# Optimization experiments

Measured on AMD Instinct MI355X. Metric: run time of the kernel, lower is better.

Reference implementation:

```python
import jax, jax.numpy as jnp
import numpy as np

NUM_HEADS = 16

def _div_no_nan(num, den):
    # TF divide_no_nan semantics: 0 where denominator is 0
    safe = jnp.where(den == 0, 1.0, den)
    return jnp.where(den == 0, 0.0, num / safe)

def setup_inputs() -> dict:
    key = jax.random.key(0)
    x = jax.random.normal(key, (8, 4096, 1024), dtype=jnp.float32)
    return {"x": x}

def reference(x) -> jnp.ndarray:
    B, S, D = x.shape
    H = NUM_HEADS
    hs = D // H
    # [B, S, H, hs] -> [B, H, S, hs]
    t = x.reshape(B, S, H, hs).transpose(0, 2, 1, 3)
    # count_nonzero over the sequence axis (axis=2 here == axis=1 inside _pca)
    non_zeros = jnp.sum((t != 0).astype(jnp.float32), axis=2, keepdims=True)      # [B,H,1,hs]
    zero_vectors = (jnp.sum((t != 0), axis=-1, keepdims=True) > 0).astype(jnp.float32)  # [B,H,S,1]
    mean_vector = _div_no_nan(jnp.sum(t, axis=2, keepdims=True), non_zeros)       # [B,H,1,hs]
    var_vector = jnp.sum(_div_no_nan(jnp.square(t - mean_vector), non_zeros), axis=2, keepdims=True)
    std_vector = jnp.sqrt(var_vector)                                             # [B,H,1,hs]
    out = _div_no_nan(t - mean_vector, std_vector) * zero_vectors                 # [B,H,S,hs]
    # Gram matrix per (batch, head): [B,H,hs,hs]
    gram = jnp.einsum('bhsi,bhsj->bhij', out, out)
    eigen_values, eigen_vectors = jnp.linalg.eigh(gram)      # [B,H,hs], [B,H,hs,hs]
    # diag(w) @ V then transpose the last two axes
    pca = jnp.swapaxes(eigen_values[..., :, None] * eigen_vectors, -1, -2)        # [B,H,hs,hs]
    pca = pca.reshape(B, H * hs, hs)
    return pca / jnp.sqrt(jnp.asarray(hs, dtype=jnp.float32))
```

## Files before the change

### kernel.cpp

```cpp
#include <hip/hip_runtime.h>
#include <math.h>


#define NMAT 128
#define EPS32 5.9604644775390625e-8
#define SAFMIN32 1.1754943508222875e-38

static __device__ __forceinline__ double f32r(double x) { return (double)(float)x; }
static __device__ __forceinline__ double lapsign(double a, double b) {
  return (b >= 0.0) ? fabs(a) : -fabs(a);
}

__device__ __forceinline__ double wred_sum(double v) {
#pragma unroll
  for (int o = 32; o > 0; o >>= 1) v += __shfl_xor(v, o, 64);
  return v;
}
__device__ __forceinline__ double wred_max(double v) {
#pragma unroll
  for (int o = 32; o > 0; o >>= 1) v = fmax(v, __shfl_xor(v, o, 64));
  return v;
}

__global__ __launch_bounds__(256) void gram_kernel(const float* __restrict__ x,
                                                   float* __restrict__ gbuf) {
  const int bh = blockIdx.x, b = bh >> 4, h = bh & 15;
  const float* base = x + (size_t)b * 4096 * 1024 + h * 64;
  __shared__ double rs1[16][64];
  __shared__ double rs2[16][64];
  __shared__ int rsc[16][64];
  __shared__ float sm[64], si[64];
  __shared__ double tiled[2][64][68];
  const int tid = threadIdx.x, q = tid & 15, r0 = tid >> 4, lane = tid & 63;

  double s1[4] = {0.0, 0.0, 0.0, 0.0}, s2[4] = {0.0, 0.0, 0.0, 0.0};
  int cc[4] = {0, 0, 0, 0};
#pragma unroll 4
  for (int s = r0; s < 4096; s += 16) {
    const float4 v = *(const float4*)&base[(size_t)s * 1024 + 4 * q];
    const float vs[4] = {v.x, v.y, v.z, v.w};
#pragma unroll
    for (int k = 0; k < 4; ++k) {
      const double dv = (double)vs[k];
      s1[k] += dv;
      s2[k] += dv * dv;
      cc[k] += (vs[k] != 0.0f) ? 1 : 0;
    }
  }
#pragma unroll
  for (int k = 0; k < 4; ++k) {
    rs1[r0][4 * q + k] = s1[k];
    rs2[r0][4 * q + k] = s2[k];
    rsc[r0][4 * q + k] = cc[k];
  }
  __syncthreads();
  if (tid < 64) {
    double S1 = 0.0, S2 = 0.0;
    int C = 0;
    for (int a = 0; a < 16; ++a) { S1 += rs1[a][tid]; S2 += rs2[a][tid]; C += rsc[a][tid]; }
    const double m = (C > 0) ? S1 / (double)C : 0.0;
    double var = (C > 0) ? (S2 - 2.0 * m * S1 + 4096.0 * m * m) / (double)C : 0.0;
    var = fmax(var, 0.0);
    const double sd = sqrt(var);
    sm[tid] = (float)m;
    si[tid] = (sd > 0.0) ? (float)(1.0 / sd) : 0.0f;
  }
  __syncthreads();

  const float4 mj4 = *(const float4*)&sm[4 * q];
  const float4 iv4 = *(const float4*)&si[4 * q];

  auto stash = [&](int buf, const float4& v, int sl) {
    const bool nz4 = (v.x != 0.0f) || (v.y != 0.0f) || (v.z != 0.0f) || (v.w != 0.0f);
    const unsigned long long mb = __ballot(nz4);
    const unsigned rowm = (unsigned)(mb >> (lane & 48)) & 0xFFFFu;
    double* tr = &tiled[buf][sl][4 * q];
    if (rowm) {
      tr[0] = (double)((v.x - mj4.x) * iv4.x);
      tr[1] = (double)((v.y - mj4.y) * iv4.y);
      tr[2] = (double)((v.z - mj4.z) * iv4.z);
      tr[3] = (double)((v.w - mj4.w) * iv4.w);
    } else {
      tr[0] = 0.0; tr[1] = 0.0; tr[2] = 0.0; tr[3] = 0.0;
    }
  };

  double acc[4][4];
#pragma unroll
  for (int r = 0; r < 4; ++r)
#pragma unroll
    for (int c = 0; c < 4; ++c) acc[r][c] = 0.0;

  {
    const float4 p0 = *(const float4*)&base[(size_t)(r0) * 1024 + 4 * q];
    const float4 p1 = *(const float4*)&base[(size_t)(r0 + 16) * 1024 + 4 * q];
    const float4 p2 = *(const float4*)&base[(size_t)(r0 + 32) * 1024 + 4 * q];
    const float4 p3 = *(const float4*)&base[(size_t)(r0 + 48) * 1024 + 4 * q];
    stash(0, p0, r0); stash(0, p1, r0 + 16); stash(0, p2, r0 + 32); stash(0, p3, r0 + 48);
  }
  __syncthreads();

  for (int t = 0; t < 64; ++t) {
    const int cur = t & 1;
    float4 n0, n1, n2, n3;
    const bool more = (t + 1 < 64);
    if (more) {
      const size_t sb = (size_t)(t + 1) * 64;
      n0 = *(const float4*)&base[(sb + r0) * 1024 + 4 * q];
      n1 = *(const float4*)&base[(sb + r0 + 16) * 1024 + 4 * q];
      n2 = *(const float4*)&base[(sb + r0 + 32) * 1024 + 4 * q];
      n3 = *(const float4*)&base[(sb + r0 + 48) * 1024 + 4 * q];
    }
    for (int ss = 0; ss < 64; ++ss) {
      const double* ta = &tiled[cur][ss][4 * r0];
      const double* tb = &tiled[cur][ss][4 * q];
      const double a0 = ta[0], a1 = ta[1], a2 = ta[2], a3 = ta[3];
      const double b0 = tb[0], b1 = tb[1], b2 = tb[2], b3 = tb[3];
      acc[0][0] += a0 * b0; acc[0][1] += a0 * b1; acc[0][2] += a0 * b2; acc[0][3] += a0 * b3;
      acc[1][0] += a1 * b0; acc[1][1] += a1 * b1; acc[1][2] += a1 * b2; acc[1][3] += a1 * b3;
      acc[2][0] += a2 * b0; acc[2][1] += a2 * b1; acc[2][2] += a2 * b2; acc[2][3] += a2 * b3;
      acc[3][0] += a3 * b0; acc[3][1] += a3 * b1; acc[3][2] += a3 * b2; acc[3][3] += a3 * b3;
    }
    if (more) {
      stash(cur ^ 1, n0, r0); stash(cur ^ 1, n1, r0 + 16);
      stash(cur ^ 1, n2, r0 + 32); stash(cur ^ 1, n3, r0 + 48);
    }
    __syncthreads();
  }

  float* G = gbuf + (size_t)bh * 4096;
#pragma unroll
  for (int r = 0; r < 4; ++r)
#pragma unroll
    for (int c = 0; c < 4; ++c)
      G[(4 * r0 + r) * 64 + 4 * q + c] = (float)acc[r][c];
}

static __device__ void dlartg_d(double f, double g, double& cs, double& sn,
                                double& r) {
  if (g == 0.0) { cs = 1.0; sn = 0.0; r = f; }
  else if (f == 0.0) { cs = 0.0; sn = 1.0; r = g; }
  else {
    r = sqrt(f * f + g * g);
    cs = f / r; sn = g / r;
    if (fabs(f) > fabs(g) && cs < 0.0) { cs = -cs; sn = -sn; r = -r; }
  }
}

static __device__ void dlaev2_d(double a, double b, double c, double& rt1,
                                double& rt2, double& cs1, double& sn1) {
  double sm = a + c, df = a - c, adf = fabs(df), tb = b + b, ab = fabs(tb);
  double acmx, acmn;
  if (fabs(a) > fabs(c)) { acmx = a; acmn = c; } else { acmx = c; acmn = a; }
  double rt;
  if (adf > ab) rt = adf * sqrt(1.0 + (ab / adf) * (ab / adf));
  else if (adf < ab) rt = ab * sqrt(1.0 + (adf / ab) * (adf / ab));
  else rt = ab * sqrt(2.0);
  int sgn1;
  if (sm < 0.0) {
    rt1 = 0.5 * (sm - rt); sgn1 = -1;
    rt2 = (acmx / rt1) * acmn - (b / rt1) * b;
  } else if (sm > 0.0) {
    rt1 = 0.5 * (sm + rt); sgn1 = 1;
    rt2 = (acmx / rt1) * acmn - (b / rt1) * b;
  } else { rt1 = 0.5 * rt; rt2 = -0.5 * rt; sgn1 = 1; }
  int sgn2; double cs;
  if (df >= 0.0) { cs = df + rt; sgn2 = 1; } else { cs = df - rt; sgn2 = -1; }
  double acs = fabs(cs);
  if (acs > ab) {
    double ct = -tb / cs;
    sn1 = 1.0 / sqrt(1.0 + ct * ct); cs1 = ct * sn1;
  } else {
    if (ab == 0.0) { cs1 = 1.0; sn1 = 0.0; }
    else {
      double tn = -cs / tb;
      cs1 = 1.0 / sqrt(1.0 + tn * tn); sn1 = tn * cs1;
    }
  }
  if (sgn1 == sgn2) { double tn = cs1; cs1 = -sn1; sn1 = tn; }
}

static __device__ void dsteqr16_grp(double (*Zs)[65], int base, int lane,
                                    double& dk, double& ek) {
  const int n = 16, nm1 = 15;
  const double eps = EPS32, eps2 = EPS32 * EPS32;
  const int gb = lane & 48;
  const int row = lane & 15;
  int l1 = 0, jtot = 0, nmaxit = n * 30;
  while (l1 < n) {
    if (l1 > 0) { if (row == l1 - 1) ek = 0.0; }
    int m;
    {
      double dkp1 = __shfl(dk, gb + ((row + 1) & 15));
      bool cond = (fabs(ek) <= (sqrt(fabs(dk)) * sqrt(fabs(dkp1))) * eps);
      unsigned grp = (unsigned)((__ballot(cond) >> gb) & 0xFFFFull);
      grp &= 0x7FFFu & ~((1u << l1) - 1);
      m = grp ? (__ffs(grp) - 1) : nm1;
      if (m < nm1) { if (row == m) ek = 0.0; }
    }
    int l = l1, lend = m;
    l1 = m + 1;
    if (lend == l) continue;
    if (fabs(__shfl(dk, gb + lend)) < fabs(__shfl(dk, gb + l))) {
      int t = l; l = lend; lend = t;
    }
    if (lend > l) {
      for (;;) {
        int mm;
        {
          double dkp1 = __shfl(dk, gb + ((row + 1) & 15));
          bool cond = (ek * ek <= (eps2 * fabs(dk)) * fabs(dkp1) + SAFMIN32);
          unsigned grp = (unsigned)((__ballot(cond) >> gb) & 0xFFFFull);
          unsigned rng = ((1u << lend) - 1) & ~((1u << l) - 1);
          grp &= rng;
          mm = grp ? (__ffs(grp) - 1) : lend;
        }
        if (mm < lend) { if (row == mm) ek = 0.0; }
        double p = __shfl(dk, gb + l);
        if (mm == l) { ++l; if (l <= lend) continue; else break; }
        if (mm == l + 1) {
          double rt1, rt2, c, s;
          dlaev2_d(__shfl(dk, gb + l), __shfl(ek, gb + l),
                   __shfl(dk, gb + l + 1), rt1, rt2, c, s);
          {
            double a = Zs[base + row][base + l], b = Zs[base + row][base + l + 1];
            Zs[base + row][base + l] = c * a + s * b;
            Zs[base + row][base + l + 1] = -s * a + c * b;
          }
          if (row == l) { dk = rt1; ek = 0.0; }
          if (row == l + 1) dk = rt2;
          l += 2; if (l <= lend) continue; else break;
        }
        if (jtot == nmaxit) break;
        ++jtot;
        double el = __shfl(ek, gb + l);
        double g = (__shfl(dk, gb + l + 1) - p) / (2.0 * el);
        double r = sqrt(g * g + 1.0);
        g = __shfl(dk, gb + mm) - p + el / (g + lapsign(r, g));
        double s = 1.0, c = 1.0; p = 0.0;
        double carry = 0.0;
        bool first = true;
        for (int i = mm - 1; i >= l; --i) {
          double za = Zs[base + row][base + i];
          double ei = __shfl(ek, gb + i);
          double f = s * ei, b = c * ei;
          dlartg_d(g, f, c, s, r);
          if (i != mm - 1) { if (row == i + 1) ek = r; }
          g = __shfl(dk, gb + i + 1) - p;
          r = (__shfl(dk, gb + i) - g) * s + 2.0 * c * b;
          p = s * r;
          if (row == i + 1) dk = g + p;
          g = c * r - b;
          double zb = first ? Zs[base + row][base + i + 1] : carry;
          Zs[base + row][base + i + 1] = s * za + c * zb;
          carry = c * za - s * zb;
          first = false;
        }
        Zs[base + row][base + l] = carry;
        if (row == l) { dk -= p; ek = g; }
      }
    } else {
      for (;;) {
        int mm;
        {
          int lm1 = (row == 0) ? 0 : row - 1;
          double dkm1 = __shfl(dk, gb + lm1);
          double ekm1 = __shfl(ek, gb + lm1);
          bool cond = (ekm1 * ekm1 <= (eps2 * fabs(dk)) * fabs(dkm1) + SAFMIN32);
          unsigned grp = (unsigned)((__ballot(cond) >> gb) & 0xFFFFull);
          unsigned rng = ((1u << (l + 1)) - 1) & ~((1u << (lend + 1)) - 1);
          grp &= rng;
          mm = grp ? (31 - __clz(grp)) : lend;
        }
        if (mm > lend) { if (row == mm - 1) ek = 0.0; }
        double p = __shfl(dk, gb + l);
        if (mm == l) { --l; if (l >= lend) continue; else break; }
        if (mm == l - 1) {
          double rt1, rt2, c, s;
          dlaev2_d(__shfl(dk, gb + l - 1), __shfl(ek, gb + l - 1),
                   __shfl(dk, gb + l), rt1, rt2, c, s);
          {
            double a = Zs[base + row][base + l - 1], b = Zs[base + row][base + l];
            Zs[base + row][base + l - 1] = c * a + s * b;
            Zs[base + row][base + l] = -s * a + c * b;
          }
          if (row == l - 1) { dk = rt1; ek = 0.0; }
          if (row == l) dk = rt2;
          l -= 2; if (l >= lend) continue; else break;
        }
        if (jtot == nmaxit) break;
        ++jtot;
        double elm1 = __shfl(ek, gb + l - 1);
        double g = (__shfl(dk, gb + l - 1) - p) / (2.0 * elm1);
        double r = sqrt(g * g + 1.0);
        g = __shfl(dk, gb + mm) - p + elm1 / (g + lapsign(r, g));
        double s = 1.0, c = 1.0; p = 0.0;
        double carry = 0.0;
        bool first = true;
        for (int i = mm; i <= l - 1; ++i) {
          double zb = Zs[base + row][base + i + 1];
          double ei = __shfl(ek, gb + i);
          double f = s * ei, b = c * ei;
          dlartg_d(g, f, c, s, r);
          if (i != mm) { if (row == i - 1) ek = r; }
          g = __shfl(dk, gb + i) - p;
          r = (__shfl(dk, gb + i + 1) - g) * s + 2.0 * c * b;
          p = s * r;
          if (row == i) dk = g + p;
          g = c * r - b;
          double za = first ? Zs[base + row][base + i] : carry;
          Zs[base + row][base + i] = c * za + s * zb;
          carry = -s * za + c * zb;
          first = false;
        }
        Zs[base + row][base + l] = carry;
        if (row == l) dk -= p;
        if (row == l - 1) ek = g;
      }
    }
  }
  for (int ii = 1; ii < n; ++ii) {
    int i = ii - 1;
    double p = __shfl(dk, gb + i);
    double mv = (row >= ii) ? dk : 1.0e300;
    mv = fmin(mv, __shfl_xor(mv, 8));
    mv = fmin(mv, __shfl_xor(mv, 4));
    mv = fmin(mv, __shfl_xor(mv, 2));
    mv = fmin(mv, __shfl_xor(mv, 1));
    if (mv < p) {
      unsigned grp = (unsigned)((__ballot(row >= ii && dk == mv) >> gb) & 0xFFFFull);
      int k = __ffs(grp) - 1;
      double dko = __shfl(dk, gb + k);
      if (row == k) dk = p;
      if (row == i) dk = dko;
      double t = Zs[base + row][base + i];
      Zs[base + row][base + i] = Zs[base + row][base + k];
      Zs[base + row][base + k] = t;
    }
  }
}

static __device__ void merge_dc(int off, int n, double rho_in, int lane,
                                double (*Zs)[65], double (*Zn)[65], float* ScF,
                                double* dd, double* dlam, double* wz,
                                double* zt, double* lamv, double* zloc,
                                double* dloc, double* lamfin, double* dvalS,
                                double* rz2, int* indx, int* slist, int* dlist,
                                int* dcolS) {
  const int N1 = n / 2;
  if (lane < n) {
    int r = (lane < N1) ? (off + N1 - 1) : (off + N1);
    double z = Zs[r][off + lane];
    if (rho_in < 0.0 && lane >= N1) z = -z;
    zloc[lane] = z * 0.70710678118654752440;
    dloc[lane] = dd[off + lane];
  }
  __syncthreads();
  const double rho = fabs(2.0 * rho_in);
  if (lane < n) {
    double a = dloc[lane];
    int pos;
    if (lane < N1) {
      int c2 = 0;
      for (int i = N1; i < n; ++i) c2 += (dloc[i] < a) ? 1 : 0;
      pos = lane + c2;
    } else {
      int c1 = 0;
      for (int i = 0; i < N1; ++i) c1 += (dloc[i] <= a) ? 1 : 0;
      pos = (lane - N1) + c1;
    }
    indx[pos] = lane;
  }
  __syncthreads();
  double mx = (lane < n) ? fmax(fabs(dloc[lane]), fabs(zloc[lane])) : 0.0;
  mx = wred_max(mx);
  const double tol = 8.0 * EPS32 * mx;
  __syncthreads();

  int K = 0, nD = 0;
  {
    int pj = -1, j = 0;
    for (; j < n; ++j) {
      int cj = indx[j];
      if (rho * fabs(zloc[cj]) <= tol) { dlist[nD] = cj; ++nD; }
      else { pj = cj; ++j; break; }
    }
    if (pj >= 0) {
      for (; j < n; ++j) {
        int nj = indx[j];
        if (rho * fabs(zloc[nj]) <= tol) { dlist[nD] = nj; ++nD; continue; }
        double s0 = zloc[pj], c0 = zloc[nj];
        double ta = sqrt(c0 * c0 + s0 * s0);
        double tt = dloc[nj] - dloc[pj];
        double cc = c0 / ta, ss = -s0 / ta;
        if (fabs(tt * cc * ss) <= tol) {
          zloc[nj] = ta; zloc[pj] = 0.0;
          {
            double a = Zs[lane][off + pj], b = Zs[lane][off + nj];
            Zs[lane][off + pj] = cc * a + ss * b;
            Zs[lane][off + nj] = cc * b - ss * a;
          }
          double ndp = dloc[pj] * cc * cc + dloc[nj] * ss * ss;
          dloc[nj] = dloc[pj] * ss * ss + dloc[nj] * cc * cc;
          dloc[pj] = ndp;
          dlist[nD] = pj; ++nD;
          pj = nj;
        } else {
          slist[K] = pj; ++K;
          pj = nj;
        }
      }
      slist[K] = pj; ++K;
    }
  }
  __syncthreads();
  if (lane == 0) {
    for (int m = 0; m < nD; ++m) { dvalS[m] = dloc[dlist[m]]; dcolS[m] = dlist[m]; }
    for (int a = 1; a < nD; ++a) {
      double v = dvalS[a]; int ci = dcolS[a]; int b = a - 1;
      while (b >= 0 && dvalS[b] > v) { dvalS[b+1] = dvalS[b]; dcolS[b+1] = dcolS[b]; --b; }
      dvalS[b+1] = v; dcolS[b+1] = ci;
    }
  }
  __syncthreads();
  if (lane < K) {
    const double dv = dloc[slist[lane]], zv = zloc[slist[lane]];
    dlam[lane] = dv; wz[lane] = zv; rz2[lane] = rho * (zv * zv);
  }
  __syncthreads();

  if (lane < K) {
    int jl = lane, pjp; double lo, hi;
    double sumz2 = 0.0;
    for (int i = 0; i < K; ++i) sumz2 += wz[i] * wz[i];
    if (jl < K - 1) {
      double mid = 0.5 * (dlam[jl] + dlam[jl + 1]);
      double f = 1.0;
      for (int i = 0; i < K; ++i) f += rho * wz[i] * wz[i] / (dlam[i] - mid);
      double gaph = 0.5 * (dlam[jl + 1] - dlam[jl]);
      if (f > 0.0) { pjp = jl;     lo = 0.0;   hi = gaph; }
      else         { pjp = jl + 1; lo = -gaph; hi = 0.0;  }
    } else { pjp = K - 1; lo = 0.0; hi = rho * sumz2; }
    double sig = dlam[pjp];
    double tau = 0.5 * (lo + hi);
    for (int it = 0; it < 100; ++it) {
      double g = 1.0, gp = 0.0;
      for (int i = 0; i < K; ++i) {
        double inv = 1.0 / ((dlam[i] - sig) - tau);
        double q = rz2[i] * inv;
        g += q;
        gp += q * inv;
      }
      if (g > 0.0) hi = tau; else lo = tau;
      double tn = tau - g / gp;
      if (!(tn > lo && tn < hi)) tn = 0.5 * (lo + hi);
      double df = fabs(tn - tau);
      tau = tn;
      if (df <= 1.0e-12 * (fabs(tau) + 1e-30)) break;
    }
    lamv[jl] = sig + tau;
    for (int i = 0; i < K; ++i)
      ScF[i * 65 + jl] = (float)((dlam[i] - sig) - tau);
  }
  __syncthreads();
  if (lane < K) {
    int i = lane;
    double wv = (double)ScF[i * 65 + i];
    for (int j2 = 0; j2 < K; ++j2) {
      if (j2 == i) continue;
      wv *= (double)ScF[i * 65 + j2] / (dlam[i] - dlam[j2]);
    }
    double mag = sqrt(fmax(-wv, 0.0));
    zt[i] = (wz[i] >= 0.0) ? mag : -mag;
  }
  __syncthreads();
  if (lane < K) {
    double nrm2 = 0.0;
    for (int i = 0; i < K; ++i) {
      double sv = zt[i] / (double)ScF[i * 65 + lane];
      ScF[i * 65 + lane] = (float)sv;
      nrm2 += sv * sv;
    }
    float inv = (float)(1.0 / sqrt(nrm2));
    for (int i = 0; i < K; ++i) ScF[i * 65 + lane] *= inv;
  }
  __syncthreads();
  if (lane < K) {
    int cnt = 0;
    for (int m = 0; m < nD; ++m) cnt += (dvalS[m] < lamv[lane]) ? 1 : 0;
    int fp = lane + cnt;
    for (int c0 = 0; c0 < n; c0 += 16) {
      double res[16];
#pragma unroll
      for (int t = 0; t < 16; ++t) res[t] = 0.0;
      for (int i = 0; i < K; ++i) {
        double sv = (double)ScF[i * 65 + lane];
        int col = off + slist[i];
#pragma unroll
        for (int t = 0; t < 16; ++t) res[t] += Zs[off + c0 + t][col] * sv;
      }
#pragma unroll
      for (int t = 0; t < 16; ++t) Zn[c0 + t][fp] = res[t];
    }
    lamfin[fp] = lamv[lane];
  }
  __syncthreads();
  for (int m = 0; m < nD; ++m) {
    int cnt = 0;
    for (int jl = 0; jl < K; ++jl) cnt += (lamv[jl] <= dvalS[m]) ? 1 : 0;
    int fp = m + cnt;
    if (lane < n) Zn[lane][fp] = Zs[off + lane][off + dcolS[m]];
    if (lane == 0) lamfin[fp] = dvalS[m];
  }
  __syncthreads();
  if (lane < n) {
    for (int c = 0; c < n; ++c) Zs[off + lane][off + c] = Zn[lane][c];
    dd[off + lane] = f32r(lamfin[lane]);
  }
  __syncthreads();
}

__global__ __launch_bounds__(64, 1) void eig_kernel(float* __restrict__ gbuf) {
  const int bh = blockIdx.x, b = bh >> 4, h = bh & 15;
  const int lane = threadIdx.x;
  float* G = gbuf + (size_t)bh * 4096;

  __shared__ double Zs[64][65];
  __shared__ double Zn[64][65];
  __shared__ double varch[64][64];
  __shared__ double ScD[2080];
  __shared__ double dd[64], ee[64], tauv[64], varr[64], wv[64];
  __shared__ double dlam[64], wz[64], zt[64], lamv[64], zloc[64], dloc[64];
  __shared__ double lamfin[64], dvalS[64], dsave[64], esave[64], rz2[64];
  __shared__ int indx[64], slist[64], dlist[64], dcolS[64];
  float* ScF = (float*)ScD;

  double (*Zw)[65] = Zs;
  for (int r = 0; r < 64; ++r) Zw[r][lane] = (double)G[r * 64 + lane];
  __syncthreads();

  for (int i = 0; i < 63; ++i) {
    double xv = (lane >= i + 2) ? Zw[i][lane] : 0.0;
    double xn2 = wred_sum(xv * xv);
    double alpha = Zw[i][i + 1];
    double beta, taui;
    if (xn2 == 0.0) { taui = 0.0; beta = alpha; }
    else {
      double nrm = sqrt(alpha * alpha + xn2);
      beta = (alpha >= 0.0) ? -nrm : nrm;
      taui = (beta - alpha) / beta;
    }
    if (lane == 0) { dd[i] = Zw[i][i]; ee[i] = beta; tauv[i] = taui; }
    if (taui != 0.0) {
      double vl = (lane == i + 1) ? 1.0
                                  : ((lane >= i + 2) ? xv / (alpha - beta) : 0.0);
      varr[lane] = vl;
      if (lane >= i + 1) varch[i][lane] = vl;
      __syncthreads();
      double wr = 0.0;
      for (int c = i + 1; c < 64; ++c) wr += Zw[c][lane] * varr[c];
      wr *= taui;
      double wtv = wred_sum((lane >= i + 1) ? wr * vl : 0.0);
      wr -= 0.5 * taui * wtv * vl;
      wv[lane] = (lane >= i + 1) ? wr : 0.0;
      __syncthreads();
      if (lane >= i + 1) {
        double vc = vl, wc = wr;
        for (int r = i + 1; r < 64; ++r)
          Zw[r][lane] -= (varr[r] * wc + wv[r] * vc);
      }
      __syncthreads();
    } else {
      __syncthreads();
    }
  }
  if (lane == 0) dd[63] = Zw[63][63];
  __syncthreads();

  dd[lane] = f32r(dd[lane]);
  if (lane < 63) ee[lane] = f32r(ee[lane]);
  __syncthreads();
  double mx = fabs(dd[lane]);
  if (lane < 63) mx = fmax(mx, fabs(ee[lane]));
  const double orgnrm = wred_max(mx);
  dd[lane] = f32r(dd[lane] / orgnrm);
  if (lane < 63) ee[lane] = f32r(ee[lane] / orgnrm);
  __syncthreads();
  dsave[lane] = dd[lane];
  esave[lane] = (lane < 63) ? ee[lane] : 0.0;
  __syncthreads();
  if (lane == 0) {
    const int ms[3] = {15, 31, 47};
    for (int a = 0; a < 3; ++a) {
      double ae = fabs(ee[ms[a]]);
      dd[ms[a]] = f32r(dd[ms[a]] - ae);
      dd[ms[a] + 1] = f32r(dd[ms[a] + 1] - ae);
    }
  }
  __syncthreads();

  for (int r = 0; r < 64; ++r) Zs[r][lane] = (r == lane) ? 1.0 : 0.0;
  __syncthreads();
  {
    const int bb = lane >> 4, row16 = lane & 15;
    double dk = dd[bb * 16 + row16];
    double ek = (row16 < 15) ? ee[bb * 16 + row16] : 0.0;
    dsteqr16_grp(Zs, bb * 16, lane, dk, ek);
    dd[bb * 16 + row16] = dk;
  }
  __syncthreads();
  dd[lane] = f32r(dd[lane]);
  __syncthreads();

  merge_dc(0, 32, ee[15], lane, Zs, Zn, ScF, dd, dlam, wz, zt, lamv, zloc,
           dloc, lamfin, dvalS, rz2, indx, slist, dlist, dcolS);
  merge_dc(32, 32, ee[47], lane, Zs, Zn, ScF, dd, dlam, wz, zt, lamv, zloc,
           dloc, lamfin, dvalS, rz2, indx, slist, dlist, dcolS);
  merge_dc(0, 64, ee[31], lane, Zs, Zn, ScF, dd, dlam, wz, zt, lamv, zloc,
           dloc, lamfin, dvalS, rz2, indx, slist, dlist, dcolS);

  double tres = 0.0;
  {
    const double lam = dd[lane];
    for (int i = 0; i < 64; ++i) {
      double tv = dsave[i] * Zs[i][lane];
      if (i > 0) tv += esave[i - 1] * Zs[i - 1][lane];
      if (i < 63) tv += esave[i] * Zs[i + 1][lane];
      tres = fmax(tres, fabs(tv - lam * Zs[i][lane]));
    }
  }
  tres = wred_max(tres);
  const bool dc_bad = !(tres <= 2e-5);

  for (int i = 62; i >= 0; --i) {
    double ti = tauv[i];
    if (ti != 0.0) {
      varr[lane] = varch[i][lane];
      __syncthreads();
      double wc = 0.0;
      for (int r = i + 1; r < 64; ++r) wc += varr[r] * Zs[r][lane];
      wc *= ti;
      for (int r = i + 1; r < 64; ++r) Zs[r][lane] -= varr[r] * wc;
      __syncthreads();
    }
  }
  __syncthreads();

  const double sentinel = dc_bad ? 1.0e6 : 0.0;
  const double wj = dd[lane] * orgnrm * 0.125;
  for (int i2 = 0; i2 < 64; ++i2) {
    G[i2 * 64 + lane] = (float)(wj * Zs[lane][i2] + sentinel);
  }
}

extern "C" void kernel_launch(void* const* d_in, const int* in_sizes, int n_in,
                              void* d_out, int out_size, void* d_ws,
                              size_t ws_size, hipStream_t stream) {
  (void)in_sizes; (void)n_in; (void)out_size; (void)d_ws; (void)ws_size;
  const float* x = (const float*)d_in[0];
  float* out = (float*)d_out;
  gram_kernel<<<dim3(NMAT), dim3(256), 0, stream>>>(x, out);
  eig_kernel<<<dim3(NMAT), dim3(64), 0, stream>>>(out);
}
```

Measured before the change: 1.683 ms.

## Run eigensolver with four wavefronts and merge independent sub-problems concurrently

Result: no change. 1.651 ms (-1.9%).

```diff
diff --git a/kernel.cpp b/kernel.cpp
--- a/kernel.cpp
+++ b/kernel.cpp
@@ -5,6 +5,10 @@
 #define NMAT 128
 #define EPS32 5.9604644775390625e-8
 #define SAFMIN32 1.1754943508222875e-38
+#define MERGE_BARRIERS 12
+
+#define WSYNC() do { asm volatile("s_waitcnt lgkmcnt(0)" ::: "memory"); \
+                     __builtin_amdgcn_sched_barrier(0); } while (0)
 
 static __device__ __forceinline__ double f32r(double x) { return (double)(float)x; }
 static __device__ __forceinline__ double lapsign(double a, double b) {
@@ -500,7 +504,7 @@
         for (int t = 0; t < 16; ++t) res[t] += Zs[off + c0 + t][col] * sv;
       }
 #pragma unroll
-      for (int t = 0; t < 16; ++t) Zn[c0 + t][fp] = res[t];
+      for (int t = 0; t < 16; ++t) Zn[off + c0 + t][off + fp] = res[t];
     }
     lamfin[fp] = lamv[lane];
   }
@@ -509,20 +513,25 @@
     int cnt = 0;
     for (int jl = 0; jl < K; ++jl) cnt += (lamv[jl] <= dvalS[m]) ? 1 : 0;
     int fp = m + cnt;
-    if (lane < n) Zn[lane][fp] = Zs[off + lane][off + dcolS[m]];
+    if (lane < n) Zn[off + lane][off + fp] = Zs[off + lane][off + dcolS[m]];
     if (lane == 0) lamfin[fp] = dvalS[m];
   }
   __syncthreads();
   if (lane < n) {
-    for (int c = 0; c < n; ++c) Zs[off + lane][off + c] = Zn[lane][c];
+    for (int c = 0; c < n; ++c) Zs[off + lane][off + c] = Zn[off + lane][off + c];
     dd[off + lane] = f32r(lamfin[lane]);
   }
   __syncthreads();
 }
 
-__global__ __launch_bounds__(64, 1) void eig_kernel(float* __restrict__ gbuf) {
-  const int bh = blockIdx.x, b = bh >> 4, h = bh & 15;
-  const int lane = threadIdx.x;
+static __device__ __forceinline__ void merge_stub() {
+#pragma unroll
+  for (int k = 0; k < MERGE_BARRIERS; ++k) __syncthreads();
+}
+
+__global__ __launch_bounds__(256, 1) void eig_kernel(float* __restrict__ gbuf) {
+  const int bh = blockIdx.x;
+  const int tid = threadIdx.x, lane = tid & 63, w = tid >> 6;
   float* G = gbuf + (size_t)bh * 4096;
 
   __shared__ double Zs[64][65];
@@ -532,123 +541,143 @@
   __shared__ double dd[64], ee[64], tauv[64], varr[64], wv[64];
   __shared__ double dlam[64], wz[64], zt[64], lamv[64], zloc[64], dloc[64];
   __shared__ double lamfin[64], dvalS[64], dsave[64], esave[64], rz2[64];
+  __shared__ double pbuf[4][64];
+  __shared__ double s_org;
   __shared__ int indx[64], slist[64], dlist[64], dcolS[64];
   float* ScF = (float*)ScD;
 
   double (*Zw)[65] = Zs;
-  for (int r = 0; r < 64; ++r) Zw[r][lane] = (double)G[r * 64 + lane];
-  __syncthreads();
-
-  for (int i = 0; i < 63; ++i) {
-    double xv = (lane >= i + 2) ? Zw[i][lane] : 0.0;
-    double xn2 = wred_sum(xv * xv);
-    double alpha = Zw[i][i + 1];
-    double beta, taui;
-    if (xn2 == 0.0) { taui = 0.0; beta = alpha; }
-    else {
-      double nrm = sqrt(alpha * alpha + xn2);
-      beta = (alpha >= 0.0) ? -nrm : nrm;
-      taui = (beta - alpha) / beta;
-    }
-    if (lane == 0) { dd[i] = Zw[i][i]; ee[i] = beta; tauv[i] = taui; }
-    if (taui != 0.0) {
-      double vl = (lane == i + 1) ? 1.0
-                                  : ((lane >= i + 2) ? xv / (alpha - beta) : 0.0);
-      varr[lane] = vl;
-      if (lane >= i + 1) varch[i][lane] = vl;
-      __syncthreads();
-      double wr = 0.0;
-      for (int c = i + 1; c < 64; ++c) wr += Zw[c][lane] * varr[c];
-      wr *= taui;
-      double wtv = wred_sum((lane >= i + 1) ? wr * vl : 0.0);
-      wr -= 0.5 * taui * wtv * vl;
-      wv[lane] = (lane >= i + 1) ? wr : 0.0;
-      __syncthreads();
-      if (lane >= i + 1) {
-        double vc = vl, wc = wr;
-        for (int r = i + 1; r < 64; ++r)
-          Zw[r][lane] -= (varr[r] * wc + wv[r] * vc);
-      }
-      __syncthreads();
-    } else {
-      __syncthreads();
-    }
-  }
-  if (lane == 0) dd[63] = Zw[63][63];
-  __syncthreads();
-
-  dd[lane] = f32r(dd[lane]);
-  if (lane < 63) ee[lane] = f32r(ee[lane]);
-  __syncthreads();
-  double mx = fabs(dd[lane]);
-  if (lane < 63) mx = fmax(mx, fabs(ee[lane]));
-  const double orgnrm = wred_max(mx);
-  dd[lane] = f32r(dd[lane] / orgnrm);
-  if (lane < 63) ee[lane] = f32r(ee[lane] / orgnrm);
-  __syncthreads();
-  dsave[lane] = dd[lane];
-  esave[lane] = (lane < 63) ? ee[lane] : 0.0;
-  __syncthreads();
-  if (lane == 0) {
-    const int ms[3] = {15, 31, 47};
-    for (int a = 0; a < 3; ++a) {
-      double ae = fabs(ee[ms[a]]);
-      dd[ms[a]] = f32r(dd[ms[a]] - ae);
-      dd[ms[a] + 1] = f32r(dd[ms[a] + 1] - ae);
-    }
-  }
-  __syncthreads();
-
-  for (int r = 0; r < 64; ++r) Zs[r][lane] = (r == lane) ? 1.0 : 0.0;
+  for (int r = 16 * w; r < 16 * w + 16; ++r) Zw[r][lane] = (double)G[r * 64 + lane];
+  __syncthreads();
+
+  if (w == 0) {
+    for (int i = 0; i < 63; ++i) {
+      double xv = (lane >= i + 2) ? Zw[i][lane] : 0.0;
+      double xn2 = wred_sum(xv * xv);
+      double alpha = Zw[i][i + 1];
+      double beta, taui;
+      if (xn2 == 0.0) { taui = 0.0; beta = alpha; }
+      else {
+        double nrm = sqrt(alpha * alpha + xn2);
+        beta = (alpha >= 0.0) ? -nrm : nrm;
+        taui = (beta - alpha) / beta;
+      }
+      if (lane == 0) { dd[i] = Zw[i][i]; ee[i] = beta; tauv[i] = taui; }
+      if (taui != 0.0) {
+        double vl = (lane == i + 1) ? 1.0
+                                    : ((lane >= i + 2) ? xv / (alpha - beta) : 0.0);
+        varr[lane] = vl;
+        if (lane >= i + 1) varch[i][lane] = vl;
+        WSYNC();
+        double wr = 0.0;
+        for (int c = i + 1; c < 64; ++c) wr += Zw[c][lane] * varr[c];
+        wr *= taui;
+        double wtv = wred_sum((lane >= i + 1) ? wr * vl : 0.0);
+        wr -= 0.5 * taui * wtv * vl;
+        wv[lane] = (lane >= i + 1) ? wr : 0.0;
+        WSYNC();
+        if (lane >= i + 1) {
+          double vc = vl, wc = wr;
+          for (int r = i + 1; r < 64; ++r)
+            Zw[r][lane] -= (varr[r] * wc + wv[r] * vc);
+        }
+        WSYNC();
+      }
+    }
+    if (lane == 0) dd[63] = Zw[63][63];
+  }
+  __syncthreads();
+
+  if (w == 0) {
+    dd[lane] = f32r(dd[lane]);
+    if (lane < 63) ee[lane] = f32r(ee[lane]);
+    double mx = fabs(dd[lane]);
+    if (lane < 63) mx = fmax(mx, fabs(ee[lane]));
+    const double orgnrm = wred_max(mx);
+    if (lane == 0) s_org = orgnrm;
+    dd[lane] = f32r(dd[lane] / orgnrm);
+    if (lane < 63) ee[lane] = f32r(ee[lane] / orgnrm);
+    dsave[lane] = dd[lane];
+    esave[lane] = (lane < 63) ? ee[lane] : 0.0;
+    WSYNC();
+    if (lane == 0) {
+      const int ms[3] = {15, 31, 47};
+      for (int a = 0; a < 3; ++a) {
+        double ae = fabs(ee[ms[a]]);
+        dd[ms[a]] = f32r(dd[ms[a]] - ae);
+        dd[ms[a] + 1] = f32r(dd[ms[a] + 1] - ae);
+      }
+    }
+  }
+  __syncthreads();
+
+  for (int r = 16 * w; r < 16 * w + 16; ++r) Zs[r][lane] = (r == lane) ? 1.0 : 0.0;
   __syncthreads();
   {
-    const int bb = lane >> 4, row16 = lane & 15;
-    double dk = dd[bb * 16 + row16];
-    double ek = (row16 < 15) ? ee[bb * 16 + row16] : 0.0;
-    dsteqr16_grp(Zs, bb * 16, lane, dk, ek);
-    dd[bb * 16 + row16] = dk;
-  }
-  __syncthreads();
-  dd[lane] = f32r(dd[lane]);
-  __syncthreads();
-
-  merge_dc(0, 32, ee[15], lane, Zs, Zn, ScF, dd, dlam, wz, zt, lamv, zloc,
-           dloc, lamfin, dvalS, rz2, indx, slist, dlist, dcolS);
-  merge_dc(32, 32, ee[47], lane, Zs, Zn, ScF, dd, dlam, wz, zt, lamv, zloc,
-           dloc, lamfin, dvalS, rz2, indx, slist, dlist, dcolS);
-  merge_dc(0, 64, ee[31], lane, Zs, Zn, ScF, dd, dlam, wz, zt, lamv, zloc,
-           dloc, lamfin, dvalS, rz2, indx, slist, dlist, dcolS);
-
-  double tres = 0.0;
+    const int row16 = lane & 15;
+    double dk = dd[16 * w + row16];
+    double ek = (row16 < 15) ? ee[16 * w + row16] : 0.0;
+    dsteqr16_grp(Zs, 16 * w, lane, dk, ek);
+    dd[16 * w + row16] = dk;
+  }
+  __syncthreads();
+  if (w == 0) dd[lane] = f32r(dd[lane]);
+  __syncthreads();
+
+  if (w == 0) {
+    merge_dc(0, 32, ee[15], lane, Zs, Zn, ScF, dd, dlam, wz, zt, lamv, zloc,
+             dloc, lamfin, dvalS, rz2, indx, slist, dlist, dcolS);
+  } else if (w == 1) {
+    merge_dc(32, 32, ee[47], lane, Zs, Zn, ScF + 32 * 65, dd, dlam + 32,
+             wz + 32, zt + 32, lamv + 32, zloc + 32, dloc + 32, lamfin + 32,
+             dvalS + 32, rz2 + 32, indx + 32, slist + 32, dlist + 32,
+             dcolS + 32);
+  } else {
+    merge_stub();
+  }
+  if (w == 0) {
+    merge_dc(0, 64, ee[31], lane, Zs, Zn, ScF, dd, dlam, wz, zt, lamv, zloc,
+             dloc, lamfin, dvalS, rz2, indx, slist, dlist, dcolS);
+  } else {
+    merge_stub();
+  }
+
   {
+    double tresp = 0.0;
     const double lam = dd[lane];
-    for (int i = 0; i < 64; ++i) {
+    for (int i = 16 * w; i < 16 * w + 16; ++i) {
       double tv = dsave[i] * Zs[i][lane];
       if (i > 0) tv += esave[i - 1] * Zs[i - 1][lane];
       if (i < 63) tv += esave[i] * Zs[i + 1][lane];
-      tres = fmax(tres, fabs(tv - lam * Zs[i][lane]));
-    }
-  }
+      tresp = fmax(tresp, fabs(tv - lam * Zs[i][lane]));
+    }
+    pbuf[w][lane] = tresp;
+  }
+  __syncthreads();
+  double tres = fmax(fmax(pbuf[0][lane], pbuf[1][lane]),
+                     fmax(pbuf[2][lane], pbuf[3][lane]));
   tres = wred_max(tres);
   const bool dc_bad = !(tres <= 2e-5);
 
-  for (int i = 62; i >= 0; --i) {
-    double ti = tauv[i];
-    if (ti != 0.0) {
-      varr[lane] = varch[i][lane];
-      __syncthreads();
-      double wc = 0.0;
-      for (int r = i + 1; r < 64; ++r) wc += varr[r] * Zs[r][lane];
-      wc *= ti;
-      for (int r = i + 1; r < 64; ++r) Zs[r][lane] -= varr[r] * wc;
-      __syncthreads();
+  if (w == 0) {
+    for (int i = 62; i >= 0; --i) {
+      double ti = tauv[i];
+      if (ti != 0.0) {
+        varr[lane] = varch[i][lane];
+        WSYNC();
+        double wc = 0.0;
+        for (int r = i + 1; r < 64; ++r) wc += varr[r] * Zs[r][lane];
+        wc *= ti;
+        for (int r = i + 1; r < 64; ++r) Zs[r][lane] -= varr[r] * wc;
+        WSYNC();
+      }
     }
   }
   __syncthreads();
 
   const double sentinel = dc_bad ? 1.0e6 : 0.0;
-  const double wj = dd[lane] * orgnrm * 0.125;
-  for (int i2 = 0; i2 < 64; ++i2) {
+  const double wj = dd[lane] * s_org * 0.125;
+  for (int i2 = 16 * w; i2 < 16 * w + 16; ++i2) {
     G[i2 * 64 + lane] = (float)(wj * Zs[lane][i2] + sentinel);
   }
 }
@@ -660,5 +689,5 @@
   const float* x = (const float*)d_in[0];
   float* out = (float*)d_out;
   gram_kernel<<<dim3(NMAT), dim3(256), 0, stream>>>(x, out);
-  eig_kernel<<<dim3(NMAT), dim3(64), 0, stream>>>(out);
-}
+  eig_kernel<<<dim3(NMAT), dim3(256), 0, stream>>>(out);
+}
```
